# Kernel optimization log

Hardware: AMD Instinct MI355X
Metric: run time of the kernel (lower is better)

## Reference

```python
import jax, jax.numpy as jnp
from jax import lax
import numpy as np

ANCHOR_LENGTHS = (2.0, 4.0, 6.0, 9.0, 13.0, 18.0)  # A = 6


def make_anchors_1d(Lf, anchor_lengths):
    # anchors on the feature axis: [Lf*A, 2] (start, end)
    al = jnp.asarray(anchor_lengths, dtype=jnp.float32)          # [A]
    centers = jnp.arange(Lf, dtype=jnp.float32) + 0.5            # [Lf]
    start = centers[:, None] - 0.5 * al[None, :]                 # [Lf, A]
    end = centers[:, None] + 0.5 * al[None, :]                   # [Lf, A]
    return jnp.stack([start, end], axis=-1).reshape(Lf * al.shape[0], 2)


def setup_inputs() -> dict:
    key = jax.random.key(0)
    ks = jax.random.split(key, 4)
    B, C, Lf, A = 4, 512, 8192, len(ANCHOR_LENGTHS)
    feat = jax.random.normal(ks[0], (B, C, Lf), dtype=jnp.float32)
    conv_w = jax.random.normal(ks[1], (C, C, 3), dtype=jnp.float32) * 0.02   # OIW
    conv_b = jnp.zeros((C,), dtype=jnp.float32)
    obj_w = jax.random.normal(ks[2], (A, C, 1), dtype=jnp.float32) * 0.02
    obj_b = jnp.zeros((A,), dtype=jnp.float32)
    reg_w = jax.random.normal(ks[3], (A * 2, C, 1), dtype=jnp.float32) * 0.02
    reg_b = jnp.zeros((A * 2,), dtype=jnp.float32)
    return {"feat": feat, "conv_w": conv_w, "conv_b": conv_b,
            "obj_w": obj_w, "obj_b": obj_b, "reg_w": reg_w, "reg_b": reg_b}


def reference(feat, conv_w, conv_b, obj_w, obj_b, reg_w, reg_b):
    B, C, Lf = feat.shape
    A = obj_w.shape[0]
    # 3x1 conv, padding=1 -> SAME; layout N C W / O I W
    h = lax.conv_general_dilated(feat, conv_w, window_strides=(1,),
                                 padding="SAME",
                                 dimension_numbers=("NCH", "OIH", "NCH"))
    h = jax.nn.relu(h + conv_b[None, :, None])                   # [B, C, Lf]
    # 1x1 conv heads expressed as channel contractions
    obj = jnp.einsum("bcl,ac->bal", h, obj_w[:, :, 0]) + obj_b[None, :, None]   # [B, A, Lf]
    reg = jnp.einsum("bcl,ac->bal", h, reg_w[:, :, 0]) + reg_b[None, :, None]   # [B, 2A, Lf]
    obj = obj.transpose(0, 2, 1).reshape(B, Lf * A)                              # [B, N]
    reg = reg.transpose(0, 2, 1).reshape(B, Lf, A, 2).reshape(B, Lf * A, 2)      # [B, N, 2]
    anchors = make_anchors_1d(Lf, ANCHOR_LENGTHS)                                # [N, 2]
    return obj, reg, anchors
```

## Files before the change

### kernel.cpp

```cpp
#include <hip/hip_runtime.h>
#include <stdint.h>

typedef __attribute__((ext_vector_type(8))) short short8;
typedef __attribute__((ext_vector_type(4))) float f32x4;
typedef __attribute__((ext_vector_type(4))) unsigned short u16x4;
typedef __attribute__((ext_vector_type(8))) unsigned short u16x8;

#define AS1 __attribute__((address_space(1)))
#define AS3 __attribute__((address_space(3)))


__device__ __forceinline__ unsigned short f2bf(float f) {
    union { float f; unsigned int u; } v; v.f = f;
    unsigned int r = v.u + 0x7fffu + ((v.u >> 16) & 1u);
    return (unsigned short)(r >> 16);
}

__constant__ float c_AL[6] = {2.f, 4.f, 6.f, 9.f, 13.f, 18.f};

__global__ __launch_bounds__(256) void prep_kernel(
    const float* __restrict__ conv_w, const float* __restrict__ obj_w,
    const float* __restrict__ reg_w, unsigned short* __restrict__ wA,
    unsigned short* __restrict__ hwp, unsigned short* __restrict__ featT,
    float* __restrict__ anchors_out) {
    int idx = blockIdx.x * 256 + threadIdx.x;
    if (idx < 786432) {
        int cout = idx / 1536, rem = idx - cout * 1536;
        int t = rem >> 9, cin = rem & 511;
        wA[idx] = f2bf(conv_w[(cout * 512 + cin) * 3 + t]);
    } else if (idx < 802816) {
        int i2 = idx - 786432;
        int j = i2 >> 9, c = i2 & 511;
        float v = 0.f;
        if (j < 6) v = obj_w[j * 512 + c];
        else if (j < 18) v = reg_w[(j - 6) * 512 + c];
        hwp[i2] = f2bf(v);
    } else if (idx < 851968) {
        int n = idx - 802816;
        int l = n / 6, a = n - l * 6;
        float ctr = (float)l + 0.5f, half = 0.5f * c_AL[a];
        anchors_out[2 * n]     = ctr - half;
        anchors_out[2 * n + 1] = ctr + half;
    } else {
        int i4 = idx - 851968;
        int b = i4 >> 10, rem = i4 & 1023;
        int row = (rem >> 9) ? 8193 : 0;
        int c = rem & 511;
        featT[((size_t)b * 8208 + row) * 512 + c] = 0;
    }
}

__global__ __launch_bounds__(256) void transpose_kernel(
    const float* __restrict__ feat, unsigned short* __restrict__ featT) {
    __shared__ float tile[64][65];
    int tid = threadIdx.x;
    int l0 = blockIdx.x * 64, c0 = blockIdx.y * 64, b = blockIdx.z;
    const float* fb = feat + ((size_t)b * 512 + c0) * 8192 + l0;
    #pragma unroll
    for (int it = 0; it < 16; ++it) {
        int slot = it * 256 + tid;
        int c = slot >> 6, l = slot & 63;
        tile[c][l] = fb[(size_t)c * 8192 + l];
    }
    __syncthreads();
    unsigned short* ftb = featT + ((size_t)b * 8208 + 1 + l0) * 512 + c0;
    #pragma unroll
    for (int it = 0; it < 16; ++it) {
        int slot = it * 256 + tid;
        int l = slot >> 6, c = slot & 63;
        ftb[(size_t)l * 512 + c] = f2bf(tile[c][l]);
    }
}

__global__ __launch_bounds__(256, 2) void conv_gemm_kernel(
    const unsigned short* __restrict__ wA,
    const unsigned short* __restrict__ featT,
    const float* __restrict__ conv_b,
    unsigned short* __restrict__ h) {
    __shared__ unsigned short smem[17408];
    unsigned short* At = smem;
    unsigned short* Bt = smem + 12288;

    const int tid = threadIdx.x;
    const int wave = tid >> 6, lane = tid & 63;
    const int lq = lane >> 4, lr = lane & 15;
    const int l0 = blockIdx.x * 128;
    const int m0 = blockIdx.y * 128;
    const int b = blockIdx.z;
    const int wm = wave >> 1, wn = wave & 1;
    const unsigned short* ftb = featT + (size_t)b * 8208 * 512;
    const int grow = lane >> 2;
    const int gcol = (lane & 3) * 8;

    f32x4 acc[4][4];
    #pragma unroll
    for (int i = 0; i < 4; ++i)
        #pragma unroll
        for (int j = 0; j < 4; ++j)
            acc[i][j] = (f32x4){0.f, 0.f, 0.f, 0.f};

    for (int kc = 0; kc < 16; ++kc) {
        __syncthreads();
        for (int ci = wave; ci < 33; ci += 4) {
            const unsigned short* g;
            if (ci < 24) {
                int t = ci >> 3, rb = ci & 7;
                g = wA + (size_t)(m0 + rb * 16 + grow) * 1536 + t * 512 + kc * 32 + gcol;
            } else {
                int cb = ci - 24;
                g = ftb + (size_t)(l0 + cb * 16 + grow) * 512 + kc * 32 + gcol;
            }
            __builtin_amdgcn_global_load_lds((const AS1 void*)g,
                                             (AS3 void*)(smem + ci * 512), 16, 0, 0);
        }
        __syncthreads();
        #pragma unroll
        for (int t = 0; t < 3; ++t) {
            short8 af[4], bf[4];
            #pragma unroll
            for (int fm = 0; fm < 4; ++fm)
                af[fm] = *(const short8*)(At + (t * 128 + wm * 64 + fm * 16 + lr) * 32 + lq * 8);
            #pragma unroll
            for (int fn = 0; fn < 4; ++fn)
                bf[fn] = *(const short8*)(Bt + (wn * 64 + fn * 16 + lr + t) * 32 + lq * 8);
            #pragma unroll
            for (int fm = 0; fm < 4; ++fm)
                #pragma unroll
                for (int fn = 0; fn < 4; ++fn)
                    acc[fm][fn] = __builtin_amdgcn_mfma_f32_16x16x32_bf16(
                        af[fm], bf[fn], acc[fm][fn], 0, 0, 0);
        }
    }
    __syncthreads();
    #pragma unroll
    for (int fm = 0; fm < 4; ++fm) {
        int mb = wm * 64 + fm * 16 + lq * 4;
        float cb0 = conv_b[m0 + mb];
        float cb1 = conv_b[m0 + mb + 1];
        float cb2 = conv_b[m0 + mb + 2];
        float cb3 = conv_b[m0 + mb + 3];
        #pragma unroll
        for (int fn = 0; fn < 4; ++fn) {
            int n = wn * 64 + fn * 16 + lr;
            f32x4 v = acc[fm][fn];
            u16x4 pk;
            pk.x = f2bf(fmaxf(v.x + cb0, 0.f));
            pk.y = f2bf(fmaxf(v.y + cb1, 0.f));
            pk.z = f2bf(fmaxf(v.z + cb2, 0.f));
            pk.w = f2bf(fmaxf(v.w + cb3, 0.f));
            *(u16x4*)(smem + n * 136 + mb) = pk;
        }
    }
    __syncthreads();
    unsigned short* hb = h + (((size_t)b * 8192 + l0) * 512) + m0;
    #pragma unroll
    for (int it = 0; it < 8; ++it) {
        int slot = it * 256 + tid;
        int n = slot >> 4, c16 = slot & 15;
        u16x8 val = *(const u16x8*)(smem + n * 136 + c16 * 8);
        *(u16x8*)(hb + (size_t)n * 512 + c16 * 8) = val;
    }
}

__global__ __launch_bounds__(64) void heads_kernel(
    const unsigned short* __restrict__ h,
    const unsigned short* __restrict__ hwp,
    const float* __restrict__ obj_b,
    const float* __restrict__ reg_b,
    float* __restrict__ out) {
    int lane = threadIdx.x;
    int lq = lane >> 4, lr = lane & 15;
    int lw = blockIdx.x * 64;
    f32x4 acc[4][2];
    #pragma unroll
    for (int i = 0; i < 4; ++i) {
        acc[i][0] = (f32x4){0.f, 0.f, 0.f, 0.f};
        acc[i][1] = (f32x4){0.f, 0.f, 0.f, 0.f};
    }
    for (int kk = 0; kk < 16; ++kk) {
        short8 af[4], bf[2];
        #pragma unroll
        for (int fm = 0; fm < 4; ++fm)
            af[fm] = *(const short8*)(h + (size_t)(lw + fm * 16 + lr) * 512 + kk * 32 + lq * 8);
        #pragma unroll
        for (int fn = 0; fn < 2; ++fn)
            bf[fn] = *(const short8*)(hwp + (size_t)(fn * 16 + lr) * 512 + kk * 32 + lq * 8);
        #pragma unroll
        for (int fm = 0; fm < 4; ++fm)
            #pragma unroll
            for (int fn = 0; fn < 2; ++fn)
                acc[fm][fn] = __builtin_amdgcn_mfma_f32_16x16x32_bf16(
                    af[fm], bf[fn], acc[fm][fn], 0, 0, 0);
    }
    int bidx = lw >> 13;
    int lloc = lw & 8191;
    float* outObj = out + (size_t)bidx * 49152;
    float* outReg = out + 196608 + (size_t)bidx * 98304;
    #pragma unroll
    for (int fn = 0; fn < 2; ++fn) {
        int j = fn * 16 + lr;
        float bias = 0.f;
        if (j < 6) bias = obj_b[j];
        else if (j < 18) bias = reg_b[j - 6];
        #pragma unroll
        for (int fm = 0; fm < 4; ++fm)
            #pragma unroll
            for (int r = 0; r < 4; ++r) {
                int l = lloc + fm * 16 + lq * 4 + r;
                float v = acc[fm][fn][r] + bias;
                if (j < 6) outObj[l * 6 + j] = v;
                else if (j < 18) outReg[l * 12 + (j - 6)] = v;
            }
    }
}

extern "C" void kernel_launch(void* const* d_in, const int* in_sizes, int n_in,
                              void* d_out, int out_size, void* d_ws, size_t ws_size,
                              hipStream_t stream) {
    const float* feat   = (const float*)d_in[0];
    const float* conv_w = (const float*)d_in[1];
    const float* conv_b = (const float*)d_in[2];
    const float* obj_w  = (const float*)d_in[3];
    const float* obj_b  = (const float*)d_in[4];
    const float* reg_w  = (const float*)d_in[5];
    const float* reg_b  = (const float*)d_in[6];
    float* out = (float*)d_out;
    char* ws = (char*)d_ws;
    unsigned short* wA    = (unsigned short*)(ws);
    unsigned short* hwp   = (unsigned short*)(ws + 1572864);
    unsigned short* featT = (unsigned short*)(ws + 1605632);
    unsigned short* hbuf  = (unsigned short*)(ws + 35225600);
    float* anchors = out + 589824;

    prep_kernel<<<dim3(3344), dim3(256), 0, stream>>>(conv_w, obj_w, reg_w, wA, hwp, featT, anchors);
    transpose_kernel<<<dim3(128, 8, 4), dim3(256), 0, stream>>>(feat, featT);
    conv_gemm_kernel<<<dim3(64, 4, 4), dim3(256), 0, stream>>>(wA, featT, conv_b, hbuf);
    heads_kernel<<<dim3(512), dim3(64), 0, stream>>>(hbuf, hwp, obj_b, reg_b, out);
}
```

Measured before the change: 181.1 us.

## Fuse head projections into conv GEMM epilogue with atomic accumulation

Measured after the change: 176.6 us. 2.4% less time.

```diff
diff --git a/kernel.cpp b/kernel.cpp
--- a/kernel.cpp
+++ b/kernel.cpp
@@ -3,6 +3,7 @@
 
 typedef __attribute__((ext_vector_type(8))) short short8;
 typedef __attribute__((ext_vector_type(4))) float f32x4;
+typedef __attribute__((ext_vector_type(4))) float float4v;
 typedef __attribute__((ext_vector_type(4))) unsigned short u16x4;
 typedef __attribute__((ext_vector_type(8))) unsigned short u16x8;
 
@@ -20,66 +21,84 @@
 
 __global__ __launch_bounds__(256) void prep_kernel(
     const float* __restrict__ conv_w, const float* __restrict__ obj_w,
-    const float* __restrict__ reg_w, unsigned short* __restrict__ wA,
+    const float* __restrict__ reg_w, const float* __restrict__ obj_b,
+    const float* __restrict__ reg_b, unsigned short* __restrict__ wAf,
     unsigned short* __restrict__ hwp, unsigned short* __restrict__ featT,
-    float* __restrict__ anchors_out) {
-    int idx = blockIdx.x * 256 + threadIdx.x;
-    if (idx < 786432) {
-        int cout = idx / 1536, rem = idx - cout * 1536;
-        int t = rem >> 9, cin = rem & 511;
-        wA[idx] = f2bf(conv_w[(cout * 512 + cin) * 3 + t]);
-    } else if (idx < 802816) {
-        int i2 = idx - 786432;
-        int j = i2 >> 9, c = i2 & 511;
+    float* __restrict__ out) {
+    unsigned int idx = blockIdx.x * 256 + threadIdx.x;
+    if (idx < 786432u) {
+        unsigned int chunkid = idx >> 9;
+        unsigned int within = idx & 511u;
+        unsigned int lane = within >> 3, j = within & 7u;
+        unsigned int kc = chunkid & 15u;
+        unsigned int ct = chunkid >> 4;
+        unsigned int t = ct % 3u, cb = ct / 3u;
+        unsigned int cout = cb * 16u + (lane & 15u);
+        unsigned int cin = kc * 32u + (lane >> 4) * 8u + j;
+        wAf[idx] = f2bf(conv_w[(cout * 512u + cin) * 3u + t]);
+    } else if (idx < 802816u) {
+        unsigned int i2 = idx - 786432u;
+        unsigned int j = i2 >> 9, c = i2 & 511u;
         float v = 0.f;
-        if (j < 6) v = obj_w[j * 512 + c];
-        else if (j < 18) v = reg_w[(j - 6) * 512 + c];
+        if (j < 6u) v = obj_w[j * 512u + c];
+        else if (j < 18u) v = reg_w[(j - 6u) * 512u + c];
         hwp[i2] = f2bf(v);
-    } else if (idx < 851968) {
-        int n = idx - 802816;
-        int l = n / 6, a = n - l * 6;
+    } else if (idx < 851968u) {
+        unsigned int n = idx - 802816u;
+        unsigned int l = n / 6u, a = n - l * 6u;
         float ctr = (float)l + 0.5f, half = 0.5f * c_AL[a];
-        anchors_out[2 * n]     = ctr - half;
-        anchors_out[2 * n + 1] = ctr + half;
-    } else {
-        int i4 = idx - 851968;
-        int b = i4 >> 10, rem = i4 & 1023;
-        int row = (rem >> 9) ? 8193 : 0;
-        int c = rem & 511;
+        float* anchors = out + 589824;
+        anchors[2 * n]     = ctr - half;
+        anchors[2 * n + 1] = ctr + half;
+    } else if (idx < 856064u) {
+        unsigned int i4 = idx - 851968u;
+        unsigned int b = i4 >> 10, rem = i4 & 1023u;
+        unsigned int row = (rem >> 9) ? 8193u : 0u;
+        unsigned int c = rem & 511u;
         featT[((size_t)b * 8208 + row) * 512 + c] = 0;
+    } else if (idx < 1052672u) {
+        unsigned int i = idx - 856064u;
+        out[i] = obj_b[i % 6u];
+    } else if (idx < 1445888u) {
+        unsigned int i = idx - 1052672u;
+        out[196608u + i] = reg_b[i % 12u];
     }
 }
 
 __global__ __launch_bounds__(256) void transpose_kernel(
     const float* __restrict__ feat, unsigned short* __restrict__ featT) {
-    __shared__ float tile[64][65];
+    __shared__ float tileT[64][69];
     int tid = threadIdx.x;
     int l0 = blockIdx.x * 64, c0 = blockIdx.y * 64, b = blockIdx.z;
     const float* fb = feat + ((size_t)b * 512 + c0) * 8192 + l0;
     #pragma unroll
-    for (int it = 0; it < 16; ++it) {
+    for (int it = 0; it < 4; ++it) {
         int slot = it * 256 + tid;
-        int c = slot >> 6, l = slot & 63;
-        tile[c][l] = fb[(size_t)c * 8192 + l];
+        int c = slot >> 4, l4 = (slot & 15) << 2;
+        float4v v = *(const float4v*)(fb + (size_t)c * 8192 + l4);
+        tileT[l4][c] = v.x; tileT[l4 + 1][c] = v.y;
+        tileT[l4 + 2][c] = v.z; tileT[l4 + 3][c] = v.w;
     }
     __syncthreads();
     unsigned short* ftb = featT + ((size_t)b * 8208 + 1 + l0) * 512 + c0;
     #pragma unroll
-    for (int it = 0; it < 16; ++it) {
+    for (int it = 0; it < 2; ++it) {
         int slot = it * 256 + tid;
-        int l = slot >> 6, c = slot & 63;
-        ftb[(size_t)l * 512 + c] = f2bf(tile[c][l]);
-    }
-}
-
-__global__ __launch_bounds__(256, 2) void conv_gemm_kernel(
-    const unsigned short* __restrict__ wA,
+        int l = slot >> 3, c8 = (slot & 7) << 3;
+        u16x8 pk;
+        #pragma unroll
+        for (int j = 0; j < 8; ++j) pk[j] = f2bf(tileT[l][c8 + j]);
+        *(u16x8*)(ftb + (size_t)l * 512 + c8) = pk;
+    }
+}
+
+__global__ __launch_bounds__(256, 3) void conv_gemm_kernel(
+    const unsigned short* __restrict__ wAf,
     const unsigned short* __restrict__ featT,
     const float* __restrict__ conv_b,
-    unsigned short* __restrict__ h) {
+    const unsigned short* __restrict__ hwp,
+    float* __restrict__ out) {
     __shared__ unsigned short smem[17408];
-    unsigned short* At = smem;
-    unsigned short* Bt = smem + 12288;
 
     const int tid = threadIdx.x;
     const int wave = tid >> 6, lane = tid & 63;
@@ -89,8 +108,6 @@
     const int b = blockIdx.z;
     const int wm = wave >> 1, wn = wave & 1;
     const unsigned short* ftb = featT + (size_t)b * 8208 * 512;
-    const int grow = lane >> 2;
-    const int gcol = (lane & 3) * 8;
 
     f32x4 acc[4][4];
     #pragma unroll
@@ -105,10 +122,10 @@
             const unsigned short* g;
             if (ci < 24) {
                 int t = ci >> 3, rb = ci & 7;
-                g = wA + (size_t)(m0 + rb * 16 + grow) * 1536 + t * 512 + kc * 32 + gcol;
+                g = wAf + ((size_t)(((m0 >> 4) + rb) * 3 + t) * 16 + kc) * 512 + lane * 8;
             } else {
-                int cb = ci - 24;
-                g = ftb + (size_t)(l0 + cb * 16 + grow) * 512 + kc * 32 + gcol;
+                int lb = ci - 24;
+                g = ftb + (size_t)(l0 + lb * 16 + lr) * 512 + kc * 32 + lq * 8;
             }
             __builtin_amdgcn_global_load_lds((const AS1 void*)g,
                                              (AS3 void*)(smem + ci * 512), 16, 0, 0);
@@ -119,10 +136,13 @@
             short8 af[4], bf[4];
             #pragma unroll
             for (int fm = 0; fm < 4; ++fm)
-                af[fm] = *(const short8*)(At + (t * 128 + wm * 64 + fm * 16 + lr) * 32 + lq * 8);
-            #pragma unroll
-            for (int fn = 0; fn < 4; ++fn)
-                bf[fn] = *(const short8*)(Bt + (wn * 64 + fn * 16 + lr + t) * 32 + lq * 8);
+                af[fm] = *(const short8*)(smem + ((t * 8 + wm * 4 + fm) << 9) + (lane << 3));
+            #pragma unroll
+            for (int fn = 0; fn < 4; ++fn) {
+                int R = wn * 64 + fn * 16 + lr + t;
+                bf[fn] = *(const short8*)(smem + ((24 + (R >> 4)) << 9) +
+                                          ((((lq << 4) | (R & 15))) << 3));
+            }
             #pragma unroll
             for (int fm = 0; fm < 4; ++fm)
                 #pragma unroll
@@ -152,64 +172,42 @@
         }
     }
     __syncthreads();
-    unsigned short* hb = h + (((size_t)b * 8192 + l0) * 512) + m0;
-    #pragma unroll
-    for (int it = 0; it < 8; ++it) {
-        int slot = it * 256 + tid;
-        int n = slot >> 4, c16 = slot & 15;
-        u16x8 val = *(const u16x8*)(smem + n * 136 + c16 * 8);
-        *(u16x8*)(hb + (size_t)n * 512 + c16 * 8) = val;
-    }
-}
-
-__global__ __launch_bounds__(64) void heads_kernel(
-    const unsigned short* __restrict__ h,
-    const unsigned short* __restrict__ hwp,
-    const float* __restrict__ obj_b,
-    const float* __restrict__ reg_b,
-    float* __restrict__ out) {
-    int lane = threadIdx.x;
-    int lq = lane >> 4, lr = lane & 15;
-    int lw = blockIdx.x * 64;
-    f32x4 acc[4][2];
-    #pragma unroll
-    for (int i = 0; i < 4; ++i) {
-        acc[i][0] = (f32x4){0.f, 0.f, 0.f, 0.f};
-        acc[i][1] = (f32x4){0.f, 0.f, 0.f, 0.f};
-    }
-    for (int kk = 0; kk < 16; ++kk) {
-        short8 af[4], bf[2];
-        #pragma unroll
-        for (int fm = 0; fm < 4; ++fm)
-            af[fm] = *(const short8*)(h + (size_t)(lw + fm * 16 + lr) * 512 + kk * 32 + lq * 8);
+    f32x4 hacc[2][2];
+    #pragma unroll
+    for (int i = 0; i < 2; ++i) {
+        hacc[i][0] = (f32x4){0.f, 0.f, 0.f, 0.f};
+        hacc[i][1] = (f32x4){0.f, 0.f, 0.f, 0.f};
+    }
+    const int lbase = wave * 32;
+    for (int kk = 0; kk < 4; ++kk) {
+        short8 ha[2], hb2[2];
+        #pragma unroll
+        for (int fm2 = 0; fm2 < 2; ++fm2)
+            ha[fm2] = *(const short8*)(smem + (lbase + fm2 * 16 + lr) * 136 + kk * 32 + lq * 8);
         #pragma unroll
         for (int fn = 0; fn < 2; ++fn)
-            bf[fn] = *(const short8*)(hwp + (size_t)(fn * 16 + lr) * 512 + kk * 32 + lq * 8);
-        #pragma unroll
-        for (int fm = 0; fm < 4; ++fm)
+            hb2[fn] = *(const short8*)(hwp + (size_t)(fn * 16 + lr) * 512 + m0 + kk * 32 + lq * 8);
+        #pragma unroll
+        for (int fm2 = 0; fm2 < 2; ++fm2)
             #pragma unroll
             for (int fn = 0; fn < 2; ++fn)
-                acc[fm][fn] = __builtin_amdgcn_mfma_f32_16x16x32_bf16(
-                    af[fm], bf[fn], acc[fm][fn], 0, 0, 0);
-    }
-    int bidx = lw >> 13;
-    int lloc = lw & 8191;
-    float* outObj = out + (size_t)bidx * 49152;
-    float* outReg = out + 196608 + (size_t)bidx * 98304;
+                hacc[fm2][fn] = __builtin_amdgcn_mfma_f32_16x16x32_bf16(
+                    ha[fm2], hb2[fn], hacc[fm2][fn], 0, 0, 0);
+    }
+    float* outObj = out + (size_t)b * 49152;
+    float* outReg = out + 196608 + (size_t)b * 98304;
     #pragma unroll
     for (int fn = 0; fn < 2; ++fn) {
         int j = fn * 16 + lr;
-        float bias = 0.f;
-        if (j < 6) bias = obj_b[j];
-        else if (j < 18) bias = reg_b[j - 6];
-        #pragma unroll
-        for (int fm = 0; fm < 4; ++fm)
+        if (j >= 18) continue;
+        #pragma unroll
+        for (int fm2 = 0; fm2 < 2; ++fm2)
             #pragma unroll
             for (int r = 0; r < 4; ++r) {
-                int l = lloc + fm * 16 + lq * 4 + r;
-                float v = acc[fm][fn][r] + bias;
-                if (j < 6) outObj[l * 6 + j] = v;
-                else if (j < 18) outReg[l * 12 + (j - 6)] = v;
+                int l = l0 + lbase + fm2 * 16 + lq * 4 + r;
+                float v = hacc[fm2][fn][r];
+                if (j < 6) atomicAdd(&outObj[l * 6 + j], v);
+                else atomicAdd(&outReg[l * 12 + (j - 6)], v);
             }
     }
 }
@@ -226,14 +224,12 @@
     const float* reg_b  = (const float*)d_in[6];
     float* out = (float*)d_out;
     char* ws = (char*)d_ws;
-    unsigned short* wA    = (unsigned short*)(ws);
+    unsigned short* wAf   = (unsigned short*)(ws);
     unsigned short* hwp   = (unsigned short*)(ws + 1572864);
     unsigned short* featT = (unsigned short*)(ws + 1605632);
-    unsigned short* hbuf  = (unsigned short*)(ws + 35225600);
-    float* anchors = out + 589824;
-
-    prep_kernel<<<dim3(3344), dim3(256), 0, stream>>>(conv_w, obj_w, reg_w, wA, hwp, featT, anchors);
+
+    prep_kernel<<<dim3(5648), dim3(256), 0, stream>>>(conv_w, obj_w, reg_w, obj_b,
+                                                      reg_b, wAf, hwp, featT, out);
     transpose_kernel<<<dim3(128, 8, 4), dim3(256), 0, stream>>>(feat, featT);
-    conv_gemm_kernel<<<dim3(64, 4, 4), dim3(256), 0, stream>>>(wA, featT, conv_b, hbuf);
-    heads_kernel<<<dim3(512), dim3(64), 0, stream>>>(hbuf, hwp, obj_b, reg_b, out);
-}
+    conv_gemm_kernel<<<dim3(64, 4, 4), dim3(256), 0, stream>>>(wAf, featT, conv_b, hwp, out);
+}
```
